# Optimization experiments

Hardware: AMD Instinct MI355X
Metric: run time of the kernel (lower is better)

Reference implementation:

```python
import jax, jax.numpy as jnp
import numpy as np

EPS = 1e-05
FACT = 2.0
REJECT_RATIO = 1.0
B, N1, N2 = 8, 4096, 4096


def setup_inputs() -> dict:
    key = jax.random.key(0)
    k1, k2 = jax.random.split(key)
    pc1 = jax.random.normal(k1, (B, 4, N1), dtype=jnp.float32)
    pc2 = jax.random.normal(k2, (B, 4, N2), dtype=jnp.float32)
    # homogeneous coordinates: last row is 1
    pc1 = pc1.at[:, 3, :].set(1.0)
    pc2 = pc2.at[:, 3, :].set(1.0)
    return {"pc1": pc1, "pc2": pc2}


def _rot_to_quat(R):
    # quaternion [w, x, y, z] from 3x3 rotation matrix (branchless)
    def s(x):
        return jnp.where(x >= 0, 1.0, -1.0)
    qw = 0.5 * jnp.sqrt(jnp.maximum(1.0 + R[0, 0] + R[1, 1] + R[2, 2], 1e-12))
    qx = 0.5 * jnp.sqrt(jnp.maximum(1.0 + R[0, 0] - R[1, 1] - R[2, 2], 1e-12)) * s(R[2, 1] - R[1, 2])
    qy = 0.5 * jnp.sqrt(jnp.maximum(1.0 - R[0, 0] + R[1, 1] - R[2, 2], 1e-12)) * s(R[0, 2] - R[2, 0])
    qz = 0.5 * jnp.sqrt(jnp.maximum(1.0 - R[0, 0] - R[1, 1] + R[2, 2], 1e-12)) * s(R[1, 0] - R[0, 1])
    return jnp.stack([qw, qx, qy, qz])


def _single(pc1, pc2):
    # pc1: [4, N1], pc2: [4, N2]
    p1, p2 = pc1[:3], pc2[:3]
    # squared pairwise distance via matmul-expansion trick: [N1, N2]
    d = (jnp.sum(p1 ** 2, axis=0)[:, None]
         - 2.0 * jnp.einsum('dn,dm->nm', p1, p2)
         + jnp.sum(p2 ** 2, axis=0)[None, :])
    # soft nearest neighbor: softmax over N2 of fact / clamp(d, eps)
    w = jax.nn.softmax(FACT / jnp.maximum(d, EPS), axis=1)  # [N1, N2]
    pc_nearest = jnp.einsum('cm,nm->cn', pc2, w)            # [4, N1]

    # soft outlier rejection (near-hard threshold via steep sigmoid)
    dist = jnp.linalg.norm(pc1 - pc_nearest, axis=0)        # [N1]
    mean_dist = jnp.mean(dist)
    indexor = jax.nn.sigmoid((dist - mean_dist * REJECT_RATIO - EPS) * -1e10)

    # weighted Procrustes (soft_tf); note indexor weights BOTH centred clouds
    wsum = jnp.sum(indexor)
    c2 = jnp.sum(pc_nearest[:3] * indexor, axis=-1) / wsum  # [3]
    c1 = jnp.sum(pc1[:3] * indexor, axis=-1) / wsum         # [3]
    p2c = ((pc_nearest[:3] - c2[:, None]) * indexor).T      # [N1, 3]
    p1c = ((pc1[:3] - c1[:, None]) * indexor).T             # [N1, 3]
    H = p1c.T @ p2c                                         # [3, 3]
    U, S, Vh = jnp.linalg.svd(H, full_matrices=False)
    V = Vh.T
    sign = jnp.where(jnp.linalg.det(U) * jnp.linalg.det(V) < 0, -1.0, 1.0)
    V = V * jnp.array([1.0, 1.0, 1.0]).at[2].set(sign)[None, :]  # flip 3rd column
    R = V @ U.T
    t = c2 - R @ c1
    T = jnp.zeros((4, 4), dtype=pc1.dtype)
    T = T.at[:3, :3].set(R).at[:3, 3].set(t).at[3, 3].set(1.0)
    q = _rot_to_quat(R)
    return T, q, t


def reference(pc1, pc2):
    T, q, t = jax.vmap(_single)(pc1, pc2)
    return T, q, t
```

## Files before the change

kernel.cpp:

```cpp
#include <hip/hip_runtime.h>
#include <math.h>


typedef float v2f __attribute__((ext_vector_type(2)));

constexpr int cB  = 8;
constexpr int cN1 = 4096;
constexpr int cN2 = 4096;
constexpr int cMC = 8;
constexpr int cCHUNK = cN2 / cMC;
constexpr int cNB2 = cN1 / 256;
constexpr float cEPS  = 1e-5f;
constexpr float cKK   = 0.34657359027997264f;
constexpr float cEPSK = cEPS * cKK;
constexpr float cUNSC = -1.4426950408889634f;

constexpr size_t OFF_PARTM = 0x400000;
constexpr size_t OFF_DPART = 0x500000;
constexpr size_t OFF_MPART = 0x500400;

__global__ __launch_bounds__(256) void cpnet_partial(
    const float* __restrict__ pc1, const float* __restrict__ pc2,
    float4* __restrict__ partA, float* __restrict__ partM) {
  __shared__ float xs[cCHUNK], ys[cCHUNK], zs[cCHUNK], ws[cCHUNK];
  __shared__ float comb[4][256][5];
  const int tid = threadIdx.x;
  const int lane = tid & 63, g = tid >> 6;
  const int b = blockIdx.z, c = blockIdx.y;
  const int nbase = blockIdx.x * 256;

  const float* p2b = pc2 + (size_t)b * 4 * cN2 + c * cCHUNK;
  for (int i = tid; i < cCHUNK; i += 256) {
    float x = p2b[i], y = p2b[cN2 + i], z = p2b[2 * cN2 + i];
    xs[i] = -2.0f * cKK * x;
    ys[i] = -2.0f * cKK * y;
    zs[i] = -2.0f * cKK * z;
    ws[i] = cKK * (x * x + y * y + z * z);
  }
  __syncthreads();

  const float* p1b = pc1 + (size_t)b * 4 * cN1;
  float x1[4], y1[4], z1[4], n1k[4];
#pragma unroll
  for (int k = 0; k < 4; ++k) {
    int r = nbase + k * 64 + lane;
    x1[k] = p1b[r];
    y1[k] = p1b[cN1 + r];
    z1[k] = p1b[2 * cN1 + r];
    n1k[k] = cKK * (x1[k] * x1[k] + y1[k] * y1[k] + z1[k] * z1[k]);
  }

  const v2f* xs2 = (const v2f*)xs + g * 64;
  const v2f* ys2 = (const v2f*)ys + g * 64;
  const v2f* zs2 = (const v2f*)zs + g * 64;
  const v2f* ws2 = (const v2f*)ws + g * 64;

  v2f dmin2[4];
#pragma unroll
  for (int k = 0; k < 4; ++k) dmin2[k] = (v2f){3.0e38f, 3.0e38f};
#pragma unroll 2
  for (int m = 0; m < 64; ++m) {
    v2f vx = xs2[m], vy = ys2[m], vz = zs2[m], vw = ws2[m];
#pragma unroll
    for (int k = 0; k < 4; ++k) {
      v2f dk = vx * x1[k] + (vy * y1[k] + (vz * z1[k] + (vw + n1k[k])));
      dmin2[k] = __builtin_elementwise_min(dmin2[k], dk);
    }
  }
  float M[4];
#pragma unroll
  for (int k = 0; k < 4; ++k)
    M[k] = __builtin_amdgcn_rcpf(fmaxf(fminf(dmin2[k].x, dmin2[k].y), cEPSK));

  v2f S2[4], Ax2[4], Ay2[4], Az2[4];
#pragma unroll
  for (int k = 0; k < 4; ++k) {
    S2[k] = (v2f){0.f, 0.f}; Ax2[k] = (v2f){0.f, 0.f};
    Ay2[k] = (v2f){0.f, 0.f}; Az2[k] = (v2f){0.f, 0.f};
  }
  const v2f EPS2 = {cEPSK, cEPSK};
#pragma unroll 2
  for (int m = 0; m < 64; ++m) {
    v2f vx = xs2[m], vy = ys2[m], vz = zs2[m], vw = ws2[m];
#pragma unroll
    for (int k = 0; k < 4; ++k) {
      v2f dk = vx * x1[k] + (vy * y1[k] + (vz * z1[k] + (vw + n1k[k])));
      dk = __builtin_elementwise_max(dk, EPS2);
      v2f s2v;
      s2v.x = __builtin_amdgcn_rcpf(dk.x);
      s2v.y = __builtin_amdgcn_rcpf(dk.y);
      v2f e;
      e.x = __builtin_amdgcn_exp2f(s2v.x - M[k]);
      e.y = __builtin_amdgcn_exp2f(s2v.y - M[k]);
      S2[k] += e;
      Ax2[k] += e * vx;
      Ay2[k] += e * vy;
      Az2[k] += e * vz;
    }
  }

#pragma unroll
  for (int k = 0; k < 4; ++k) {
    int r = k * 64 + lane;
    comb[g][r][0] = S2[k].x + S2[k].y;
    comb[g][r][1] = Ax2[k].x + Ax2[k].y;
    comb[g][r][2] = Ay2[k].x + Ay2[k].y;
    comb[g][r][3] = Az2[k].x + Az2[k].y;
    comb[g][r][4] = M[k];
  }
  __syncthreads();

  float m0 = comb[0][tid][4], m1 = comb[1][tid][4],
        m2 = comb[2][tid][4], m3 = comb[3][tid][4];
  float mrow = fmaxf(fmaxf(m0, m1), fmaxf(m2, m3));
  float S = 0.f, Ax = 0.f, Ay = 0.f, Az = 0.f;
#pragma unroll
  for (int gg = 0; gg < 4; ++gg) {
    float w = exp2f(comb[gg][tid][4] - mrow);
    S  += comb[gg][tid][0] * w;
    Ax += comb[gg][tid][1] * w;
    Ay += comb[gg][tid][2] * w;
    Az += comb[gg][tid][3] * w;
  }
  const int idx = (c * cB + b) * cN1 + nbase + tid;
  partA[idx] = make_float4(Ax, Ay, Az, S);
  partM[idx] = mrow;
}

__device__ __forceinline__ void reduce_multi(double* v, int nv, double* lds,
                                             int tid) {
  const int lane = tid & 63, w = tid >> 6;
  for (int i = 0; i < nv; ++i) {
    double x = v[i];
    for (int s = 32; s > 0; s >>= 1) x += __shfl_xor(x, s, 64);
    if (lane == 0) lds[i * 4 + w] = x;
  }
  __syncthreads();
  if (tid < nv)
    lds[tid * 4] = lds[tid * 4] + lds[tid * 4 + 1] + lds[tid * 4 + 2] +
                   lds[tid * 4 + 3];
  __syncthreads();
  for (int i = 0; i < nv; ++i) v[i] = lds[i * 4];
  __syncthreads();
}

__global__ __launch_bounds__(256) void cpnet_combine(
    const float* __restrict__ pc1, float4* partA,
    const float* __restrict__ partM, double* __restrict__ dpart) {
  __shared__ double lds[32 * 4];
  const int tid = threadIdx.x;
  const int bx = blockIdx.x, b = blockIdx.y;
  const int n = bx * 256 + tid;

  float Ms[cMC];
  float g = -3.0e38f;
#pragma unroll
  for (int c = 0; c < cMC; ++c) {
    Ms[c] = partM[(c * cB + b) * cN1 + n];
    g = fmaxf(g, Ms[c]);
  }
  float S = 0.f, nx = 0.f, ny = 0.f, nz = 0.f;
#pragma unroll
  for (int c = 0; c < cMC; ++c) {
    float w = exp2f(Ms[c] - g);
    float4 a = partA[(c * cB + b) * cN1 + n];
    S += a.w * w; nx += a.x * w; ny += a.y * w; nz += a.z * w;
  }
  float inv = cUNSC / S;
  nx *= inv; ny *= inv; nz *= inv;
  const float* p1b = pc1 + (size_t)b * 4 * cN1;
  float dx = p1b[n] - nx, dy = p1b[cN1 + n] - ny, dz = p1b[2 * cN1 + n] - nz;
  float dist = sqrtf(dx * dx + dy * dy + dz * dz);
  partA[(0 * cB + b) * cN1 + n] = make_float4(nx, ny, nz, dist);

  double acc[1];
  acc[0] = (double)dist;
  reduce_multi(acc, 1, lds, tid);
  if (tid == 0) dpart[b * cNB2 + bx] = acc[0];
}

__global__ __launch_bounds__(256) void cpnet_moments(
    const float* __restrict__ pc1, const float4* __restrict__ partA,
    const double* __restrict__ dpart, double* __restrict__ mpart) {
  __shared__ double lds[32 * 4];
  const int tid = threadIdx.x;
  const int bx = blockIdx.x, b = blockIdx.y;
  const int n = bx * 256 + tid;

  double dsum = 0.0;
  for (int i = 0; i < cNB2; ++i) dsum += dpart[b * cNB2 + i];
  const float meanf = (float)(dsum * (1.0 / (double)cN1));

  float4 nn = partA[(0 * cB + b) * cN1 + n];
  float u = (nn.w - meanf - cEPS) * 1e10f;
  float ind = 1.0f / (1.0f + expf(u));
  const float* p1b = pc1 + (size_t)b * 4 * cN1;
  double di = (double)ind, di2 = di * di;
  double x1 = (double)p1b[n], y1 = (double)p1b[cN1 + n],
         z1 = (double)p1b[2 * cN1 + n];
  double x2 = (double)nn.x, y2 = (double)nn.y, z2 = (double)nn.z;

  double a[23];
  a[0] = di;
  a[1] = di * x1;  a[2] = di * y1;  a[3] = di * z1;
  a[4] = di * x2;  a[5] = di * y2;  a[6] = di * z2;
  a[7] = di2;
  a[8]  = di2 * x1;  a[9]  = di2 * y1;  a[10] = di2 * z1;
  a[11] = di2 * x2;  a[12] = di2 * y2;  a[13] = di2 * z2;
  a[14] = di2 * x1 * x2; a[15] = di2 * x1 * y2; a[16] = di2 * x1 * z2;
  a[17] = di2 * y1 * x2; a[18] = di2 * y1 * y2; a[19] = di2 * y1 * z2;
  a[20] = di2 * z1 * x2; a[21] = di2 * z1 * y2; a[22] = di2 * z1 * z2;

  reduce_multi(a, 23, lds, tid);
  if (tid == 0) {
    double* mb = mpart + (size_t)(b * cNB2 + bx) * 23;
    for (int i = 0; i < 23; ++i) mb[i] = a[i];
  }
}

__global__ __launch_bounds__(64) void cpnet_solve(
    const double* __restrict__ mpart, float* __restrict__ out) {
  const int b = blockIdx.x;
  if (threadIdx.x != 0) return;

  double acc[23];
  for (int i = 0; i < 23; ++i) acc[i] = 0.0;
  for (int k = 0; k < cNB2; ++k) {
    const double* mb = mpart + (size_t)(b * cNB2 + k) * 23;
    for (int i = 0; i < 23; ++i) acc[i] += mb[i];
  }

  double W = acc[0];
  double c1[3] = {acc[1] / W, acc[2] / W, acc[3] / W};
  double c2[3] = {acc[4] / W, acc[5] / W, acc[6] / W};
  double H[3][3];
  for (int i = 0; i < 3; ++i)
    for (int j = 0; j < 3; ++j)
      H[i][j] = acc[14 + 3 * i + j] - c2[j] * acc[8 + i] -
                c1[i] * acc[11 + j] + c1[i] * c2[j] * acc[7];

  double trH = H[0][0] + H[1][1] + H[2][2];
  double Nm[4][4], V[4][4];
  Nm[0][0] = trH;
  Nm[0][1] = Nm[1][0] = H[1][2] - H[2][1];
  Nm[0][2] = Nm[2][0] = H[2][0] - H[0][2];
  Nm[0][3] = Nm[3][0] = H[0][1] - H[1][0];
  Nm[1][1] = 2.0 * H[0][0] - trH;
  Nm[1][2] = Nm[2][1] = H[0][1] + H[1][0];
  Nm[1][3] = Nm[3][1] = H[0][2] + H[2][0];
  Nm[2][2] = 2.0 * H[1][1] - trH;
  Nm[2][3] = Nm[3][2] = H[1][2] + H[2][1];
  Nm[3][3] = 2.0 * H[2][2] - trH;

  for (int i = 0; i < 4; ++i)
    for (int j = 0; j < 4; ++j) V[i][j] = (i == j) ? 1.0 : 0.0;

  for (int sweep = 0; sweep < 6; ++sweep) {
    for (int p = 0; p < 3; ++p) {
      for (int q = p + 1; q < 4; ++q) {
        double apq = Nm[p][q];
        if (fabs(apq) < 1e-300) continue;
        double theta = (Nm[q][q] - Nm[p][p]) / (2.0 * apq);
        double tt = (theta >= 0.0 ? 1.0 : -1.0) /
                    (fabs(theta) + sqrt(theta * theta + 1.0));
        double cc = 1.0 / sqrt(tt * tt + 1.0);
        double ss = tt * cc;
        for (int k = 0; k < 4; ++k) {
          double akp = Nm[k][p], akq = Nm[k][q];
          Nm[k][p] = cc * akp - ss * akq;
          Nm[k][q] = ss * akp + cc * akq;
        }
        for (int k = 0; k < 4; ++k) {
          double apk = Nm[p][k], aqk = Nm[q][k];
          Nm[p][k] = cc * apk - ss * aqk;
          Nm[q][k] = ss * apk + cc * aqk;
        }
        for (int k = 0; k < 4; ++k) {
          double vkp = V[k][p], vkq = V[k][q];
          V[k][p] = cc * vkp - ss * vkq;
          V[k][q] = ss * vkp + cc * vkq;
        }
      }
    }
  }
  int imax = 0;
  for (int i = 1; i < 4; ++i)
    if (Nm[i][i] > Nm[imax][imax]) imax = i;
  double qw = V[0][imax], qx = V[1][imax], qy = V[2][imax], qz = V[3][imax];
  double qn = sqrt(qw * qw + qx * qx + qy * qy + qz * qz);
  qw /= qn; qx /= qn; qy /= qn; qz /= qn;

  double R[3][3];
  R[0][0] = 1.0 - 2.0 * (qy * qy + qz * qz);
  R[0][1] = 2.0 * (qx * qy - qw * qz);
  R[0][2] = 2.0 * (qx * qz + qw * qy);
  R[1][0] = 2.0 * (qx * qy + qw * qz);
  R[1][1] = 1.0 - 2.0 * (qx * qx + qz * qz);
  R[1][2] = 2.0 * (qy * qz - qw * qx);
  R[2][0] = 2.0 * (qx * qz - qw * qy);
  R[2][1] = 2.0 * (qy * qz + qw * qx);
  R[2][2] = 1.0 - 2.0 * (qx * qx + qy * qy);

  double tr1 = 0.0, tr2 = 0.0;
  for (int i = 0; i < 3; ++i)
    for (int j = 0; j < 3; ++j) {
      tr1 += R[i][j] * H[j][i];
      tr2 += R[j][i] * H[j][i];
    }
  if (tr2 > tr1) {
    for (int i = 0; i < 3; ++i)
      for (int j = i + 1; j < 3; ++j) {
        double tmp = R[i][j]; R[i][j] = R[j][i]; R[j][i] = tmp;
      }
  }

  double tx = c2[0] - (R[0][0] * c1[0] + R[0][1] * c1[1] + R[0][2] * c1[2]);
  double ty = c2[1] - (R[1][0] * c1[0] + R[1][1] * c1[1] + R[1][2] * c1[2]);
  double tz = c2[2] - (R[2][0] * c1[0] + R[2][1] * c1[1] + R[2][2] * c1[2]);

  auto sgn = [](double x) { return x >= 0.0 ? 1.0 : -1.0; };
  double oqw = 0.5 * sqrt(fmax(1.0 + R[0][0] + R[1][1] + R[2][2], 1e-12));
  double oqx = 0.5 * sqrt(fmax(1.0 + R[0][0] - R[1][1] - R[2][2], 1e-12)) *
               sgn(R[2][1] - R[1][2]);
  double oqy = 0.5 * sqrt(fmax(1.0 - R[0][0] + R[1][1] - R[2][2], 1e-12)) *
               sgn(R[0][2] - R[2][0]);
  double oqz = 0.5 * sqrt(fmax(1.0 - R[0][0] - R[1][1] + R[2][2], 1e-12)) *
               sgn(R[1][0] - R[0][1]);

  float* T = out + b * 16;
  T[0]  = (float)R[0][0]; T[1]  = (float)R[0][1]; T[2]  = (float)R[0][2]; T[3]  = (float)tx;
  T[4]  = (float)R[1][0]; T[5]  = (float)R[1][1]; T[6]  = (float)R[1][2]; T[7]  = (float)ty;
  T[8]  = (float)R[2][0]; T[9]  = (float)R[2][1]; T[10] = (float)R[2][2]; T[11] = (float)tz;
  T[12] = 0.f; T[13] = 0.f; T[14] = 0.f; T[15] = 1.f;
  float* Q = out + 128 + b * 4;
  Q[0] = (float)oqw; Q[1] = (float)oqx; Q[2] = (float)oqy; Q[3] = (float)oqz;
  float* Tt = out + 160 + b * 3;
  Tt[0] = (float)tx; Tt[1] = (float)ty; Tt[2] = (float)tz;
}

extern "C" void kernel_launch(void* const* d_in, const int* in_sizes, int n_in,
                              void* d_out, int out_size, void* d_ws, size_t ws_size,
                              hipStream_t stream) {
  const float* pc1 = (const float*)d_in[0];
  const float* pc2 = (const float*)d_in[1];
  float* out = (float*)d_out;
  char* ws = (char*)d_ws;

  float4* partA = (float4*)ws;
  float*  partM = (float*)(ws + OFF_PARTM);
  double* dpart = (double*)(ws + OFF_DPART);
  double* mpart = (double*)(ws + OFF_MPART);

  cpnet_partial<<<dim3(cN1 / 256, cMC, cB), 256, 0, stream>>>(pc1, pc2,
                                                              partA, partM);
  cpnet_combine<<<dim3(cNB2, cB), 256, 0, stream>>>(pc1, partA, partM, dpart);
  cpnet_moments<<<dim3(cNB2, cB), 256, 0, stream>>>(pc1, partA, dpart, mpart);
  cpnet_solve<<<cB, 64, 0, stream>>>(mpart, out);
}
```

Baseline: 139.2 us.

## Fuse combine, moments and solve kernels into one per-batch tail kernel

Replaces the three post-processing kernels (combine, moments, solve) with a single kernel that runs one 512-thread block per batch. Each thread merges the partial softmax results for 8 points, and the block reduces the mean distance in shared memory. It then accumulates the Procrustes moments and solves in place. This removes two launches and the global round-trips through dpart/mpart, in exchange for much lower parallelism: only 8 blocks handle the whole tail.

```diff
diff --git a/kernel.cpp b/kernel.cpp
--- a/kernel.cpp
+++ b/kernel.cpp
@@ -9,15 +9,12 @@
 constexpr int cN2 = 4096;
 constexpr int cMC = 8;
 constexpr int cCHUNK = cN2 / cMC;
-constexpr int cNB2 = cN1 / 256;
 constexpr float cEPS  = 1e-5f;
 constexpr float cKK   = 0.34657359027997264f;
 constexpr float cEPSK = cEPS * cKK;
 constexpr float cUNSC = -1.4426950408889634f;
 
 constexpr size_t OFF_PARTM = 0x400000;
-constexpr size_t OFF_DPART = 0x500000;
-constexpr size_t OFF_MPART = 0x500400;
 
 __global__ __launch_bounds__(256) void cpnet_partial(
     const float* __restrict__ pc1, const float* __restrict__ pc2,
@@ -127,108 +124,97 @@
   partM[idx] = mrow;
 }
 
-__device__ __forceinline__ void reduce_multi(double* v, int nv, double* lds,
-                                             int tid) {
+__global__ __launch_bounds__(512) void cpnet_tail(
+    const float* __restrict__ pc1, const float4* __restrict__ partA,
+    const float* __restrict__ partM, float* __restrict__ out) {
+  __shared__ double lds[23 * 8];
+  __shared__ float s_mean;
+  const int tid = threadIdx.x;
   const int lane = tid & 63, w = tid >> 6;
-  for (int i = 0; i < nv; ++i) {
-    double x = v[i];
+  const int b = blockIdx.x;
+  const float* p1b = pc1 + (size_t)b * 4 * cN1;
+
+  float nxr[8], nyr[8], nzr[8], dr[8];
+  double dsum = 0.0;
+#pragma unroll
+  for (int k = 0; k < 8; ++k) {
+    const int n = k * 512 + tid;
+    float Ms[cMC];
+    float g = -3.0e38f;
+#pragma unroll
+    for (int c = 0; c < cMC; ++c) {
+      Ms[c] = partM[(c * cB + b) * cN1 + n];
+      g = fmaxf(g, Ms[c]);
+    }
+    float S = 0.f, nx = 0.f, ny = 0.f, nz = 0.f;
+#pragma unroll
+    for (int c = 0; c < cMC; ++c) {
+      float wgt = exp2f(Ms[c] - g);
+      float4 a4 = partA[(c * cB + b) * cN1 + n];
+      S += a4.w * wgt; nx += a4.x * wgt; ny += a4.y * wgt; nz += a4.z * wgt;
+    }
+    float inv = cUNSC / S;
+    nx *= inv; ny *= inv; nz *= inv;
+    float dx = p1b[n] - nx, dy = p1b[cN1 + n] - ny, dz = p1b[2 * cN1 + n] - nz;
+    float dist = sqrtf(dx * dx + dy * dy + dz * dz);
+    nxr[k] = nx; nyr[k] = ny; nzr[k] = nz; dr[k] = dist;
+    dsum += (double)dist;
+  }
+
+  {
+    double x = dsum;
     for (int s = 32; s > 0; s >>= 1) x += __shfl_xor(x, s, 64);
-    if (lane == 0) lds[i * 4 + w] = x;
-  }
-  __syncthreads();
-  if (tid < nv)
-    lds[tid * 4] = lds[tid * 4] + lds[tid * 4 + 1] + lds[tid * 4 + 2] +
-                   lds[tid * 4 + 3];
-  __syncthreads();
-  for (int i = 0; i < nv; ++i) v[i] = lds[i * 4];
-  __syncthreads();
-}
-
-__global__ __launch_bounds__(256) void cpnet_combine(
-    const float* __restrict__ pc1, float4* partA,
-    const float* __restrict__ partM, double* __restrict__ dpart) {
-  __shared__ double lds[32 * 4];
-  const int tid = threadIdx.x;
-  const int bx = blockIdx.x, b = blockIdx.y;
-  const int n = bx * 256 + tid;
-
-  float Ms[cMC];
-  float g = -3.0e38f;
-#pragma unroll
-  for (int c = 0; c < cMC; ++c) {
-    Ms[c] = partM[(c * cB + b) * cN1 + n];
-    g = fmaxf(g, Ms[c]);
-  }
-  float S = 0.f, nx = 0.f, ny = 0.f, nz = 0.f;
-#pragma unroll
-  for (int c = 0; c < cMC; ++c) {
-    float w = exp2f(Ms[c] - g);
-    float4 a = partA[(c * cB + b) * cN1 + n];
-    S += a.w * w; nx += a.x * w; ny += a.y * w; nz += a.z * w;
-  }
-  float inv = cUNSC / S;
-  nx *= inv; ny *= inv; nz *= inv;
-  const float* p1b = pc1 + (size_t)b * 4 * cN1;
-  float dx = p1b[n] - nx, dy = p1b[cN1 + n] - ny, dz = p1b[2 * cN1 + n] - nz;
-  float dist = sqrtf(dx * dx + dy * dy + dz * dz);
-  partA[(0 * cB + b) * cN1 + n] = make_float4(nx, ny, nz, dist);
-
-  double acc[1];
-  acc[0] = (double)dist;
-  reduce_multi(acc, 1, lds, tid);
-  if (tid == 0) dpart[b * cNB2 + bx] = acc[0];
-}
-
-__global__ __launch_bounds__(256) void cpnet_moments(
-    const float* __restrict__ pc1, const float4* __restrict__ partA,
-    const double* __restrict__ dpart, double* __restrict__ mpart) {
-  __shared__ double lds[32 * 4];
-  const int tid = threadIdx.x;
-  const int bx = blockIdx.x, b = blockIdx.y;
-  const int n = bx * 256 + tid;
-
-  double dsum = 0.0;
-  for (int i = 0; i < cNB2; ++i) dsum += dpart[b * cNB2 + i];
-  const float meanf = (float)(dsum * (1.0 / (double)cN1));
-
-  float4 nn = partA[(0 * cB + b) * cN1 + n];
-  float u = (nn.w - meanf - cEPS) * 1e10f;
-  float ind = 1.0f / (1.0f + expf(u));
-  const float* p1b = pc1 + (size_t)b * 4 * cN1;
-  double di = (double)ind, di2 = di * di;
-  double x1 = (double)p1b[n], y1 = (double)p1b[cN1 + n],
-         z1 = (double)p1b[2 * cN1 + n];
-  double x2 = (double)nn.x, y2 = (double)nn.y, z2 = (double)nn.z;
+    if (lane == 0) lds[w] = x;
+  }
+  __syncthreads();
+  if (tid == 0) {
+    double t = 0.0;
+    for (int i = 0; i < 8; ++i) t += lds[i];
+    s_mean = (float)(t * (1.0 / (double)cN1));
+  }
+  __syncthreads();
+  const float meanf = s_mean;
 
   double a[23];
-  a[0] = di;
-  a[1] = di * x1;  a[2] = di * y1;  a[3] = di * z1;
-  a[4] = di * x2;  a[5] = di * y2;  a[6] = di * z2;
-  a[7] = di2;
-  a[8]  = di2 * x1;  a[9]  = di2 * y1;  a[10] = di2 * z1;
-  a[11] = di2 * x2;  a[12] = di2 * y2;  a[13] = di2 * z2;
-  a[14] = di2 * x1 * x2; a[15] = di2 * x1 * y2; a[16] = di2 * x1 * z2;
-  a[17] = di2 * y1 * x2; a[18] = di2 * y1 * y2; a[19] = di2 * y1 * z2;
-  a[20] = di2 * z1 * x2; a[21] = di2 * z1 * y2; a[22] = di2 * z1 * z2;
-
-  reduce_multi(a, 23, lds, tid);
-  if (tid == 0) {
-    double* mb = mpart + (size_t)(b * cNB2 + bx) * 23;
-    for (int i = 0; i < 23; ++i) mb[i] = a[i];
-  }
-}
-
-__global__ __launch_bounds__(64) void cpnet_solve(
-    const double* __restrict__ mpart, float* __restrict__ out) {
-  const int b = blockIdx.x;
-  if (threadIdx.x != 0) return;
+  for (int i = 0; i < 23; ++i) a[i] = 0.0;
+#pragma unroll
+  for (int k = 0; k < 8; ++k) {
+    const int n = k * 512 + tid;
+    float u = (dr[k] - meanf - cEPS) * 1e10f;
+    float ind = 1.0f / (1.0f + expf(u));
+    double di = (double)ind, di2 = di * di;
+    double x1 = (double)p1b[n], y1 = (double)p1b[cN1 + n],
+           z1 = (double)p1b[2 * cN1 + n];
+    double x2 = (double)nxr[k], y2 = (double)nyr[k], z2 = (double)nzr[k];
+
+    a[0] += di;
+    a[1] += di * x1;  a[2] += di * y1;  a[3] += di * z1;
+    a[4] += di * x2;  a[5] += di * y2;  a[6] += di * z2;
+    a[7] += di2;
+    a[8]  += di2 * x1;  a[9]  += di2 * y1;  a[10] += di2 * z1;
+    a[11] += di2 * x2;  a[12] += di2 * y2;  a[13] += di2 * z2;
+    a[14] += di2 * x1 * x2; a[15] += di2 * x1 * y2; a[16] += di2 * x1 * z2;
+    a[17] += di2 * y1 * x2; a[18] += di2 * y1 * y2; a[19] += di2 * y1 * z2;
+    a[20] += di2 * z1 * x2; a[21] += di2 * z1 * y2; a[22] += di2 * z1 * z2;
+  }
+
+  for (int i = 0; i < 23; ++i) {
+    double x = a[i];
+    for (int s = 32; s > 0; s >>= 1) x += __shfl_xor(x, s, 64);
+    if (lane == 0) lds[i * 8 + w] = x;
+  }
+  __syncthreads();
+  if (tid < 23) {
+    double t = 0.0;
+    for (int j = 0; j < 8; ++j) t += lds[tid * 8 + j];
+    lds[tid * 8] = t;
+  }
+  __syncthreads();
+
+  if (tid != 0) return;
 
   double acc[23];
-  for (int i = 0; i < 23; ++i) acc[i] = 0.0;
-  for (int k = 0; k < cNB2; ++k) {
-    const double* mb = mpart + (size_t)(b * cNB2 + k) * 23;
-    for (int i = 0; i < 23; ++i) acc[i] += mb[i];
-  }
+  for (int i = 0; i < 23; ++i) acc[i] = lds[i * 8];
 
   double W = acc[0];
   double c1[3] = {acc[1] / W, acc[2] / W, acc[3] / W};
@@ -348,12 +334,8 @@
 
   float4* partA = (float4*)ws;
   float*  partM = (float*)(ws + OFF_PARTM);
-  double* dpart = (double*)(ws + OFF_DPART);
-  double* mpart = (double*)(ws + OFF_MPART);
 
   cpnet_partial<<<dim3(cN1 / 256, cMC, cB), 256, 0, stream>>>(pc1, pc2,
                                                               partA, partM);
-  cpnet_combine<<<dim3(cNB2, cB), 256, 0, stream>>>(pc1, partA, partM, dpart);
-  cpnet_moments<<<dim3(cNB2, cB), 256, 0, stream>>>(pc1, partA, dpart, mpart);
-  cpnet_solve<<<cB, 64, 0, stream>>>(mpart, out);
+  cpnet_tail<<<cB, 512, 0, stream>>>(pc1, partA, partM, out);
 }
```

Result: no change. 141.9 us (+2.0%).

## Halve rows per block in partial kernel and fuse moments with solve

Applied to the files above, without the earlier changes.

The partial-softmax kernel now covers 128 query rows per block instead of 256, with each thread handling two rows and a deeper unroll. This doubles the grid to 2048 blocks and adds an occupancy hint to the launch bounds. Separately, the moments and Procrustes solve kernels are merged into one per-batch kernel that loops over all points and reduces in-block, removing a launch and the intermediate moment buffer. The trade-off is that the 23-moment reduction now runs on only 8 blocks instead of 128, so that stage gets less parallelism.

```diff
diff --git a/kernel.cpp b/kernel.cpp
--- a/kernel.cpp
+++ b/kernel.cpp
@@ -9,6 +9,7 @@
 constexpr int cN2 = 4096;
 constexpr int cMC = 8;
 constexpr int cCHUNK = cN2 / cMC;
+constexpr int cROWS = 128;
 constexpr int cNB2 = cN1 / 256;
 constexpr float cEPS  = 1e-5f;
 constexpr float cKK   = 0.34657359027997264f;
@@ -17,17 +18,16 @@
 
 constexpr size_t OFF_PARTM = 0x400000;
 constexpr size_t OFF_DPART = 0x500000;
-constexpr size_t OFF_MPART = 0x500400;
-
-__global__ __launch_bounds__(256) void cpnet_partial(
+
+__global__ __launch_bounds__(256, 8) void cpnet_partial(
     const float* __restrict__ pc1, const float* __restrict__ pc2,
     float4* __restrict__ partA, float* __restrict__ partM) {
   __shared__ float xs[cCHUNK], ys[cCHUNK], zs[cCHUNK], ws[cCHUNK];
-  __shared__ float comb[4][256][5];
+  __shared__ float comb[4][cROWS][5];
   const int tid = threadIdx.x;
   const int lane = tid & 63, g = tid >> 6;
   const int b = blockIdx.z, c = blockIdx.y;
-  const int nbase = blockIdx.x * 256;
+  const int nbase = blockIdx.x * cROWS;
 
   const float* p2b = pc2 + (size_t)b * 4 * cN2 + c * cCHUNK;
   for (int i = tid; i < cCHUNK; i += 256) {
@@ -40,9 +40,9 @@
   __syncthreads();
 
   const float* p1b = pc1 + (size_t)b * 4 * cN1;
-  float x1[4], y1[4], z1[4], n1k[4];
-#pragma unroll
-  for (int k = 0; k < 4; ++k) {
+  float x1[2], y1[2], z1[2], n1k[2];
+#pragma unroll
+  for (int k = 0; k < 2; ++k) {
     int r = nbase + k * 64 + lane;
     x1[k] = p1b[r];
     y1[k] = p1b[cN1 + r];
@@ -55,35 +55,35 @@
   const v2f* zs2 = (const v2f*)zs + g * 64;
   const v2f* ws2 = (const v2f*)ws + g * 64;
 
-  v2f dmin2[4];
-#pragma unroll
-  for (int k = 0; k < 4; ++k) dmin2[k] = (v2f){3.0e38f, 3.0e38f};
-#pragma unroll 2
+  v2f dmin2[2];
+#pragma unroll
+  for (int k = 0; k < 2; ++k) dmin2[k] = (v2f){3.0e38f, 3.0e38f};
+#pragma unroll 4
   for (int m = 0; m < 64; ++m) {
     v2f vx = xs2[m], vy = ys2[m], vz = zs2[m], vw = ws2[m];
 #pragma unroll
-    for (int k = 0; k < 4; ++k) {
+    for (int k = 0; k < 2; ++k) {
       v2f dk = vx * x1[k] + (vy * y1[k] + (vz * z1[k] + (vw + n1k[k])));
       dmin2[k] = __builtin_elementwise_min(dmin2[k], dk);
     }
   }
-  float M[4];
-#pragma unroll
-  for (int k = 0; k < 4; ++k)
+  float M[2];
+#pragma unroll
+  for (int k = 0; k < 2; ++k)
     M[k] = __builtin_amdgcn_rcpf(fmaxf(fminf(dmin2[k].x, dmin2[k].y), cEPSK));
 
-  v2f S2[4], Ax2[4], Ay2[4], Az2[4];
-#pragma unroll
-  for (int k = 0; k < 4; ++k) {
+  v2f S2[2], Ax2[2], Ay2[2], Az2[2];
+#pragma unroll
+  for (int k = 0; k < 2; ++k) {
     S2[k] = (v2f){0.f, 0.f}; Ax2[k] = (v2f){0.f, 0.f};
     Ay2[k] = (v2f){0.f, 0.f}; Az2[k] = (v2f){0.f, 0.f};
   }
   const v2f EPS2 = {cEPSK, cEPSK};
-#pragma unroll 2
+#pragma unroll 4
   for (int m = 0; m < 64; ++m) {
     v2f vx = xs2[m], vy = ys2[m], vz = zs2[m], vw = ws2[m];
 #pragma unroll
-    for (int k = 0; k < 4; ++k) {
+    for (int k = 0; k < 2; ++k) {
       v2f dk = vx * x1[k] + (vy * y1[k] + (vz * z1[k] + (vw + n1k[k])));
       dk = __builtin_elementwise_max(dk, EPS2);
       v2f s2v;
@@ -100,7 +100,7 @@
   }
 
 #pragma unroll
-  for (int k = 0; k < 4; ++k) {
+  for (int k = 0; k < 2; ++k) {
     int r = k * 64 + lane;
     comb[g][r][0] = S2[k].x + S2[k].y;
     comb[g][r][1] = Ax2[k].x + Ax2[k].y;
@@ -110,21 +110,23 @@
   }
   __syncthreads();
 
-  float m0 = comb[0][tid][4], m1 = comb[1][tid][4],
-        m2 = comb[2][tid][4], m3 = comb[3][tid][4];
-  float mrow = fmaxf(fmaxf(m0, m1), fmaxf(m2, m3));
-  float S = 0.f, Ax = 0.f, Ay = 0.f, Az = 0.f;
-#pragma unroll
-  for (int gg = 0; gg < 4; ++gg) {
-    float w = exp2f(comb[gg][tid][4] - mrow);
-    S  += comb[gg][tid][0] * w;
-    Ax += comb[gg][tid][1] * w;
-    Ay += comb[gg][tid][2] * w;
-    Az += comb[gg][tid][3] * w;
-  }
-  const int idx = (c * cB + b) * cN1 + nbase + tid;
-  partA[idx] = make_float4(Ax, Ay, Az, S);
-  partM[idx] = mrow;
+  if (tid < cROWS) {
+    float m0 = comb[0][tid][4], m1 = comb[1][tid][4],
+          m2 = comb[2][tid][4], m3 = comb[3][tid][4];
+    float mrow = fmaxf(fmaxf(m0, m1), fmaxf(m2, m3));
+    float S = 0.f, Ax = 0.f, Ay = 0.f, Az = 0.f;
+#pragma unroll
+    for (int gg = 0; gg < 4; ++gg) {
+      float w = exp2f(comb[gg][tid][4] - mrow);
+      S  += comb[gg][tid][0] * w;
+      Ax += comb[gg][tid][1] * w;
+      Ay += comb[gg][tid][2] * w;
+      Az += comb[gg][tid][3] * w;
+    }
+    const int idx = (c * cB + b) * cN1 + nbase + tid;
+    partA[idx] = make_float4(Ax, Ay, Az, S);
+    partM[idx] = mrow;
+  }
 }
 
 __device__ __forceinline__ void reduce_multi(double* v, int nv, double* lds,
@@ -179,65 +181,52 @@
   if (tid == 0) dpart[b * cNB2 + bx] = acc[0];
 }
 
-__global__ __launch_bounds__(256) void cpnet_moments(
+__global__ __launch_bounds__(256) void cpnet_moments_solve(
     const float* __restrict__ pc1, const float4* __restrict__ partA,
-    const double* __restrict__ dpart, double* __restrict__ mpart) {
-  __shared__ double lds[32 * 4];
+    const double* __restrict__ dpart, float* __restrict__ out) {
+  __shared__ double lds[23 * 4];
   const int tid = threadIdx.x;
-  const int bx = blockIdx.x, b = blockIdx.y;
-  const int n = bx * 256 + tid;
+  const int b = blockIdx.x;
+  const float* p1b = pc1 + (size_t)b * 4 * cN1;
 
   double dsum = 0.0;
   for (int i = 0; i < cNB2; ++i) dsum += dpart[b * cNB2 + i];
   const float meanf = (float)(dsum * (1.0 / (double)cN1));
 
-  float4 nn = partA[(0 * cB + b) * cN1 + n];
-  float u = (nn.w - meanf - cEPS) * 1e10f;
-  float ind = 1.0f / (1.0f + expf(u));
-  const float* p1b = pc1 + (size_t)b * 4 * cN1;
-  double di = (double)ind, di2 = di * di;
-  double x1 = (double)p1b[n], y1 = (double)p1b[cN1 + n],
-         z1 = (double)p1b[2 * cN1 + n];
-  double x2 = (double)nn.x, y2 = (double)nn.y, z2 = (double)nn.z;
-
   double a[23];
-  a[0] = di;
-  a[1] = di * x1;  a[2] = di * y1;  a[3] = di * z1;
-  a[4] = di * x2;  a[5] = di * y2;  a[6] = di * z2;
-  a[7] = di2;
-  a[8]  = di2 * x1;  a[9]  = di2 * y1;  a[10] = di2 * z1;
-  a[11] = di2 * x2;  a[12] = di2 * y2;  a[13] = di2 * z2;
-  a[14] = di2 * x1 * x2; a[15] = di2 * x1 * y2; a[16] = di2 * x1 * z2;
-  a[17] = di2 * y1 * x2; a[18] = di2 * y1 * y2; a[19] = di2 * y1 * z2;
-  a[20] = di2 * z1 * x2; a[21] = di2 * z1 * y2; a[22] = di2 * z1 * z2;
-
+  for (int i = 0; i < 23; ++i) a[i] = 0.0;
+  for (int it = 0; it < cNB2; ++it) {
+    const int n = it * 256 + tid;
+    float4 nn = partA[(0 * cB + b) * cN1 + n];
+    float u = (nn.w - meanf - cEPS) * 1e10f;
+    float ind = 1.0f / (1.0f + expf(u));
+    double di = (double)ind, di2 = di * di;
+    double x1 = (double)p1b[n], y1 = (double)p1b[cN1 + n],
+           z1 = (double)p1b[2 * cN1 + n];
+    double x2 = (double)nn.x, y2 = (double)nn.y, z2 = (double)nn.z;
+
+    a[0] += di;
+    a[1] += di * x1;  a[2] += di * y1;  a[3] += di * z1;
+    a[4] += di * x2;  a[5] += di * y2;  a[6] += di * z2;
+    a[7] += di2;
+    a[8]  += di2 * x1;  a[9]  += di2 * y1;  a[10] += di2 * z1;
+    a[11] += di2 * x2;  a[12] += di2 * y2;  a[13] += di2 * z2;
+    a[14] += di2 * x1 * x2; a[15] += di2 * x1 * y2; a[16] += di2 * x1 * z2;
+    a[17] += di2 * y1 * x2; a[18] += di2 * y1 * y2; a[19] += di2 * y1 * z2;
+    a[20] += di2 * z1 * x2; a[21] += di2 * z1 * y2; a[22] += di2 * z1 * z2;
+  }
   reduce_multi(a, 23, lds, tid);
-  if (tid == 0) {
-    double* mb = mpart + (size_t)(b * cNB2 + bx) * 23;
-    for (int i = 0; i < 23; ++i) mb[i] = a[i];
-  }
-}
-
-__global__ __launch_bounds__(64) void cpnet_solve(
-    const double* __restrict__ mpart, float* __restrict__ out) {
-  const int b = blockIdx.x;
-  if (threadIdx.x != 0) return;
-
-  double acc[23];
-  for (int i = 0; i < 23; ++i) acc[i] = 0.0;
-  for (int k = 0; k < cNB2; ++k) {
-    const double* mb = mpart + (size_t)(b * cNB2 + k) * 23;
-    for (int i = 0; i < 23; ++i) acc[i] += mb[i];
-  }
-
-  double W = acc[0];
-  double c1[3] = {acc[1] / W, acc[2] / W, acc[3] / W};
-  double c2[3] = {acc[4] / W, acc[5] / W, acc[6] / W};
+
+  if (tid != 0) return;
+
+  double W = a[0];
+  double c1[3] = {a[1] / W, a[2] / W, a[3] / W};
+  double c2[3] = {a[4] / W, a[5] / W, a[6] / W};
   double H[3][3];
   for (int i = 0; i < 3; ++i)
     for (int j = 0; j < 3; ++j)
-      H[i][j] = acc[14 + 3 * i + j] - c2[j] * acc[8 + i] -
-                c1[i] * acc[11 + j] + c1[i] * c2[j] * acc[7];
+      H[i][j] = a[14 + 3 * i + j] - c2[j] * a[8 + i] -
+                c1[i] * a[11 + j] + c1[i] * c2[j] * a[7];
 
   double trH = H[0][0] + H[1][1] + H[2][2];
   double Nm[4][4], V[4][4];
@@ -349,11 +338,9 @@
   float4* partA = (float4*)ws;
   float*  partM = (float*)(ws + OFF_PARTM);
   double* dpart = (double*)(ws + OFF_DPART);
-  double* mpart = (double*)(ws + OFF_MPART);
-
-  cpnet_partial<<<dim3(cN1 / 256, cMC, cB), 256, 0, stream>>>(pc1, pc2,
-                                                              partA, partM);
+
+  cpnet_partial<<<dim3(cN1 / cROWS, cMC, cB), 256, 0, stream>>>(pc1, pc2,
+                                                                partA, partM);
   cpnet_combine<<<dim3(cNB2, cB), 256, 0, stream>>>(pc1, partA, partM, dpart);
-  cpnet_moments<<<dim3(cNB2, cB), 256, 0, stream>>>(pc1, partA, dpart, mpart);
-  cpnet_solve<<<cB, 64, 0, stream>>>(mpart, out);
-}
+  cpnet_moments_solve<<<cB, 256, 0, stream>>>(pc1, partA, dpart, out);
+}
```

Result: no change. 137.1 us (-1.5%).
